# Kernel optimization log

Measured on AMD Instinct MI355X. Metric: run time of the kernel, lower is better.

Reference implementation:

```python
import jax, jax.numpy as jnp
import numpy as np


def setup_inputs() -> dict:
    key = jax.random.key(0)
    k1, k2, k3 = jax.random.split(key, 3)
    B, C, H, W = 16, 512, 64, 64
    K = 32
    std = 1.0 / (K * C) ** 0.5
    x = jax.random.normal(k1, (B, C, H, W), dtype=jnp.float32)
    codewords = jax.random.uniform(k2, (K, C), dtype=jnp.float32, minval=-std, maxval=std)
    scale = jax.random.uniform(k3, (K,), dtype=jnp.float32, minval=-1.0, maxval=0.0)
    return {"x": x, "codewords": codewords, "scale": scale}


def reference(x, codewords, scale):
    # x: [B, C, H, W] -> tokens [B, N, C] with N = H*W
    B, C, H, W = x.shape
    xf = x.reshape(B, C, H * W).transpose(0, 2, 1)  # [B, N, C]

    # (avoids materializing the [B, N, K, C] tensor the torch code builds)
    x_sq = jnp.sum(xf * xf, axis=-1)                 # [B, N]
    c_sq = jnp.sum(codewords * codewords, axis=-1)   # [K]
    xc = jnp.einsum('bnc,kc->bnk', xf, codewords)    # [B, N, K]
    scaled_l2 = scale * (x_sq[..., None] - 2.0 * xc + c_sq)  # [B, N, K]

    w = jax.nn.softmax(scaled_l2, axis=2)            # [B, N, K]

    # aggregate: sum_n w[b,n,k] * (x[b,n,:] - c[k,:])
    #          = einsum(w, x) - (sum_n w) * c
    enc = jnp.einsum('bnk,bnc->bkc', w, xf) - jnp.sum(w, axis=1)[..., None] * codewords
    return enc  # [B, K, C]
```

## Files before the change

kernel.cpp:

```cpp
#include <hip/hip_runtime.h>


#define B_ 16
#define C_ 512
#define N_ 4096
#define K_ 32
#define CHUNK 64
#define NCH (N_ / CHUNK)
#define NBLK (B_ * NCH)
#define XCP 72
#define WLS 40

typedef __attribute__((ext_vector_type(8))) short short8;
typedef __attribute__((ext_vector_type(16))) float floatx16;

__device__ inline unsigned short f2bf(float f) {
    union { float f; unsigned u; } v; v.f = f;
    unsigned r = v.u + 0x7FFFu + ((v.u >> 16) & 1u);
    return (unsigned short)(r >> 16);
}

__global__ __launch_bounds__(256)
void cw_convert(const float* __restrict__ cw, unsigned short* __restrict__ cwb,
                float* __restrict__ csq)
{
    const int tid = threadIdx.x;
    const int k = tid >> 3, q = tid & 7;
    const float4* src = (const float4*)(cw + k * C_ + q * 64);
    float s = 0.f;
    #pragma unroll
    for (int i = 0; i < 16; ++i) {
        const float4 v = src[i];
        s += v.x*v.x + v.y*v.y + v.z*v.z + v.w*v.w;
        const unsigned lo = (unsigned)f2bf(v.x) | ((unsigned)f2bf(v.y) << 16);
        const unsigned hi = (unsigned)f2bf(v.z) | ((unsigned)f2bf(v.w) << 16);
        *(uint2*)&cwb[k * C_ + q * 64 + i * 4] = make_uint2(lo, hi);
    }
    s += __shfl_xor(s, 1); s += __shfl_xor(s, 2); s += __shfl_xor(s, 4);
    if (q == 0) csq[k] = s;
}

template <int USE_WS>
__global__ __launch_bounds__(256, 2)
void enc_kernel(const float* __restrict__ x,
                const unsigned short* __restrict__ cwb,
                const float* __restrict__ csqg,
                const float* __restrict__ cw,
                const float* __restrict__ scale,
                float* __restrict__ outp)
{
    __shared__ unsigned short XC[C_ * XCP];
    __shared__ unsigned short Wl[2][K_ * WLS];
    __shared__ float xsqp[4][CHUNK];
    __shared__ float csq[K_];
    __shared__ float scl[K_];

    const int tid  = threadIdx.x;
    const int wave = tid >> 6;
    const int lane = tid & 63;
    const int l31  = lane & 31;
    const int lh   = lane >> 5;

    const int b     = blockIdx.x >> 6;
    const int chunk = blockIdx.x & (NCH - 1);
    const float* xb = x + (long)b * C_ * N_;

    const int r = tid >> 4;
    const int p = tid & 15;
    const float* xrow = xb + chunk * CHUNK + p * 4;

    if (tid < K_) { scl[tid] = scale[tid]; csq[tid] = csqg[tid]; }

    float4 s0[4], s1[4], s2[4];
#define XISSUE(buf_, g_)                                                       \
    { _Pragma("unroll")                                                        \
      for (int i = 0; i < 4; ++i)                                              \
          buf_[i] = *(const float4*)(xrow + (long)((g_) * 64 + i * 16 + r) * N_); }

    float xs0 = 0.f, xs1 = 0.f, xs2 = 0.f, xs3 = 0.f;
#define XWRITE(buf_, g_)                                                       \
    { _Pragma("unroll")                                                        \
      for (int i = 0; i < 4; ++i) {                                            \
          const float4 v = buf_[i];                                            \
          xs0 += v.x * v.x; xs1 += v.y * v.y;                                  \
          xs2 += v.z * v.z; xs3 += v.w * v.w;                                  \
          const unsigned lo = (unsigned)f2bf(v.x) | ((unsigned)f2bf(v.y) << 16);\
          const unsigned hi = (unsigned)f2bf(v.z) | ((unsigned)f2bf(v.w) << 16);\
          *(uint2*)&XC[((g_) * 64 + i * 16 + r) * XCP + p * 4] = make_uint2(lo, hi);\
      } }

    const unsigned short* cwr = cwb + l31 * C_ + lh * 8;
    short8 afA[4], afB[4];
#define AFLOAD(buf_, g_)                                                       \
    { _Pragma("unroll")                                                        \
      for (int s = 0; s < 4; ++s)                                              \
          buf_[s] = *(const short8*)(cwr + (g_) * 64 + s * 16); }

    XISSUE(s0, 0)
    XISSUE(s1, 1)
    if (wave < 2) AFLOAD(afA, 0)
    XWRITE(s0, 0)
    XISSUE(s2, 2)
    __syncthreads();

    floatx16 S;
    #pragma unroll
    for (int i = 0; i < 16; ++i) S[i] = 0.f;

    #pragma unroll
    for (int g = 0; g < 8; ++g) {
        if (g + 3 < 8) {
            if      ((g % 3) == 0) XISSUE(s0, g + 3)
            else if ((g % 3) == 1) XISSUE(s1, g + 3)
            else                   XISSUE(s2, g + 3)
        }
        if (wave < 2) {
            if (g + 1 < 8) {
                if (g & 1) AFLOAD(afA, g + 1) else AFLOAD(afB, g + 1)
            }
            #pragma unroll
            for (int s = 0; s < 4; ++s) {
                short8 bx;
                #pragma unroll
                for (int j = 0; j < 8; ++j)
                    bx[j] = (short)XC[(g * 64 + s * 16 + lh * 8 + j) * XCP + wave * 32 + l31];
                S = __builtin_amdgcn_mfma_f32_32x32x16_bf16((g & 1) ? afB[s] : afA[s],
                                                            bx, S, 0, 0, 0);
            }
        }
        if (g + 1 < 8) {
            if      (((g + 1) % 3) == 0) XWRITE(s0, g + 1)
            else if (((g + 1) % 3) == 1) XWRITE(s1, g + 1)
            else                         XWRITE(s2, g + 1)
        }
        if (g < 7) __syncthreads();
    }

    xs0 += __shfl_xor(xs0, 16); xs1 += __shfl_xor(xs1, 16);
    xs2 += __shfl_xor(xs2, 16); xs3 += __shfl_xor(xs3, 16);
    xs0 += __shfl_xor(xs0, 32); xs1 += __shfl_xor(xs1, 32);
    xs2 += __shfl_xor(xs2, 32); xs3 += __shfl_xor(xs3, 32);
    if (lane < 16) {
        xsqp[wave][lane * 4 + 0] = xs0; xsqp[wave][lane * 4 + 1] = xs1;
        xsqp[wave][lane * 4 + 2] = xs2; xsqp[wave][lane * 4 + 3] = xs3;
    }
    __syncthreads();

    if (wave < 2) {
        const int n = wave * 32 + l31;
        const float xq = xsqp[0][n] + xsqp[1][n] + xsqp[2][n] + xsqp[3][n];
        float L[16], mx = -3.4e38f;
        #pragma unroll
        for (int rr = 0; rr < 16; ++rr) {
            const int k = (rr & 3) + 8 * (rr >> 2) + 4 * lh;
            L[rr] = scl[k] * (xq - 2.f * S[rr] + csq[k]);
            mx = fmaxf(mx, L[rr]);
        }
        mx = fmaxf(mx, __shfl_xor(mx, 32));
        float sum = 0.f;
        #pragma unroll
        for (int rr = 0; rr < 16; ++rr) { L[rr] = __expf(L[rr] - mx); sum += L[rr]; }
        sum += __shfl_xor(sum, 32);
        const float inv = 1.f / sum;
        #pragma unroll
        for (int rr = 0; rr < 16; ++rr) {
            const int k = (rr & 3) + 8 * (rr >> 2) + 4 * lh;
            Wl[wave][k * WLS + l31] = f2bf(L[rr] * inv);
        }
    }
    __syncthreads();

    short8 aw[4];
    #pragma unroll
    for (int s = 0; s < 4; ++s)
        aw[s] = *(const short8*)&Wl[s >> 1][l31 * WLS + (s & 1) * 16 + lh * 8];

    floatx16 wacc;
    #pragma unroll
    for (int i = 0; i < 16; ++i) wacc[i] = 0.f;
    {
        short8 ones;
        #pragma unroll
        for (int j = 0; j < 8; ++j) ones[j] = (short)0x3F80;
        #pragma unroll
        for (int s = 0; s < 4; ++s)
            wacc = __builtin_amdgcn_mfma_f32_32x32x16_bf16(aw[s], ones, wacc, 0, 0, 0);
    }

    floatx16 acc[4];
    #pragma unroll
    for (int t = 0; t < 4; ++t)
        #pragma unroll
        for (int i = 0; i < 16; ++i) acc[t][i] = 0.f;

    #pragma unroll
    for (int t = 0; t < 4; ++t) {
        const int c = wave * 128 + t * 32 + l31;
        #pragma unroll
        for (int s = 0; s < 4; ++s) {
            const short8 bx = *(const short8*)&XC[c * XCP + s * 16 + lh * 8];
            acc[t] = __builtin_amdgcn_mfma_f32_32x32x16_bf16(aw[s], bx, acc[t], 0, 0, 0);
        }
    }

    float* dst = USE_WS ? (outp + (size_t)blockIdx.x * K_ * C_)
                        : (outp + (size_t)b * K_ * C_);
    #pragma unroll
    for (int t = 0; t < 4; ++t) {
        const int c = wave * 128 + t * 32 + l31;
        #pragma unroll
        for (int rr = 0; rr < 16; ++rr) {
            const int k = (rr & 3) + 8 * (rr >> 2) + 4 * lh;
            const float val = acc[t][rr] - wacc[rr] * cw[k * C_ + c];
            if (USE_WS) dst[k * C_ + c] = val;
            else        atomicAdd(dst + k * C_ + c, val);
        }
    }
}

__global__ __launch_bounds__(256)
void reduce_kernel(const float4* __restrict__ part, float4* __restrict__ out)
{
    const int gid = blockIdx.x * 256 + threadIdx.x;
    const int bb  = gid >> 12;
    const int i4  = gid & 4095;
    const float4* p = part + ((size_t)bb * NCH) * 4096 + i4;
    float4 s = make_float4(0.f, 0.f, 0.f, 0.f);
    #pragma unroll 8
    for (int ch = 0; ch < NCH; ++ch) {
        const float4 v = p[(size_t)ch * 4096];
        s.x += v.x; s.y += v.y; s.z += v.z; s.w += v.w;
    }
    out[gid] = s;
}

extern "C" void kernel_launch(void* const* d_in, const int* in_sizes, int n_in,
                              void* d_out, int out_size, void* d_ws, size_t ws_size,
                              hipStream_t stream) {
    const float* x     = (const float*)d_in[0];
    const float* cw    = (const float*)d_in[1];
    const float* scale = (const float*)d_in[2];
    float* out = (float*)d_out;

    unsigned short* cwb = (unsigned short*)d_ws;
    float* csq = (float*)((char*)d_ws + (size_t)K_ * C_ * sizeof(unsigned short));
    const size_t part_off = 65536;
    const size_t ws_need = part_off + (size_t)NBLK * K_ * C_ * sizeof(float);

    if (ws_size >= ws_need) {
        float* part = (float*)((char*)d_ws + part_off);
        hipLaunchKernelGGL(cw_convert, dim3(1), dim3(256), 0, stream, cw, cwb, csq);
        hipLaunchKernelGGL(enc_kernel<1>, dim3(NBLK), dim3(256), 0, stream,
                           x, cwb, csq, cw, scale, part);
        hipLaunchKernelGGL(reduce_kernel, dim3(256), dim3(256), 0, stream,
                           (const float4*)part, (float4*)out);
    } else {
        hipMemsetAsync(out, 0, (size_t)out_size * sizeof(float), stream);
        hipLaunchKernelGGL(cw_convert, dim3(1), dim3(256), 0, stream, cw, cwb, csq);
        hipLaunchKernelGGL(enc_kernel<0>, dim3(NBLK), dim3(256), 0, stream,
                           x, cwb, csq, cw, scale, out);
    }
}
```

Before: 222.9 us.

## Process two token chunks per block and fold codeword conversion into main kernel

```diff
diff --git a/kernel.cpp b/kernel.cpp
--- a/kernel.cpp
+++ b/kernel.cpp
@@ -6,8 +6,9 @@
 #define N_ 4096
 #define K_ 32
 #define CHUNK 64
-#define NCH (N_ / CHUNK)
-#define NBLK (B_ * NCH)
+#define CPB 2
+#define BPB (N_ / (CHUNK * CPB))
+#define NBLK (B_ * BPB)
 #define XCP 72
 #define WLS 40
 
@@ -20,31 +21,16 @@
     return (unsigned short)(r >> 16);
 }
 
-__global__ __launch_bounds__(256)
-void cw_convert(const float* __restrict__ cw, unsigned short* __restrict__ cwb,
-                float* __restrict__ csq)
-{
-    const int tid = threadIdx.x;
-    const int k = tid >> 3, q = tid & 7;
-    const float4* src = (const float4*)(cw + k * C_ + q * 64);
-    float s = 0.f;
-    #pragma unroll
-    for (int i = 0; i < 16; ++i) {
-        const float4 v = src[i];
-        s += v.x*v.x + v.y*v.y + v.z*v.z + v.w*v.w;
-        const unsigned lo = (unsigned)f2bf(v.x) | ((unsigned)f2bf(v.y) << 16);
-        const unsigned hi = (unsigned)f2bf(v.z) | ((unsigned)f2bf(v.w) << 16);
-        *(uint2*)&cwb[k * C_ + q * 64 + i * 4] = make_uint2(lo, hi);
-    }
-    s += __shfl_xor(s, 1); s += __shfl_xor(s, 2); s += __shfl_xor(s, 4);
-    if (q == 0) csq[k] = s;
+__device__ inline void cbar() {
+    __builtin_amdgcn_sched_barrier(0);
+    asm volatile("s_waitcnt lgkmcnt(0)" ::: "memory");
+    __builtin_amdgcn_s_barrier();
+    __builtin_amdgcn_sched_barrier(0);
 }
 
 template <int USE_WS>
 __global__ __launch_bounds__(256, 2)
 void enc_kernel(const float* __restrict__ x,
-                const unsigned short* __restrict__ cwb,
-                const float* __restrict__ csqg,
                 const float* __restrict__ cw,
                 const float* __restrict__ scale,
                 float* __restrict__ outp)
@@ -61,23 +47,20 @@
     const int l31  = lane & 31;
     const int lh   = lane >> 5;
 
-    const int b     = blockIdx.x >> 6;
-    const int chunk = blockIdx.x & (NCH - 1);
+    const int b    = blockIdx.x >> 5;
+    const int pair = blockIdx.x & (BPB - 1);
     const float* xb = x + (long)b * C_ * N_;
 
     const int r = tid >> 4;
     const int p = tid & 15;
-    const float* xrow = xb + chunk * CHUNK + p * 4;
-
-    if (tid < K_) { scl[tid] = scale[tid]; csq[tid] = csqg[tid]; }
 
     float4 s0[4], s1[4], s2[4];
-#define XISSUE(buf_, g_)                                                       \
+#define XISSUE(buf_, ch_, g_)                                                  \
     { _Pragma("unroll")                                                        \
       for (int i = 0; i < 4; ++i)                                              \
-          buf_[i] = *(const float4*)(xrow + (long)((g_) * 64 + i * 16 + r) * N_); }
-
-    float xs0 = 0.f, xs1 = 0.f, xs2 = 0.f, xs3 = 0.f;
+          buf_[i] = *(const float4*)(xb + (long)((g_) * 64 + i * 16 + r) * N_  \
+                                     + (pair * CPB + (ch_)) * CHUNK + p * 4); }
+
 #define XWRITE(buf_, g_)                                                       \
     { _Pragma("unroll")                                                        \
       for (int i = 0; i < 4; ++i) {                                            \
@@ -89,118 +72,155 @@
           *(uint2*)&XC[((g_) * 64 + i * 16 + r) * XCP + p * 4] = make_uint2(lo, hi);\
       } }
 
-    const unsigned short* cwr = cwb + l31 * C_ + lh * 8;
+    const float* cwr = cw + l31 * C_ + lh * 8;
     short8 afA[4], afB[4];
-#define AFLOAD(buf_, g_)                                                       \
+#define AFLOADG(buf_, g_)                                                      \
     { _Pragma("unroll")                                                        \
-      for (int s = 0; s < 4; ++s)                                              \
-          buf_[s] = *(const short8*)(cwr + (g_) * 64 + s * 16); }
-
-    XISSUE(s0, 0)
-    XISSUE(s1, 1)
-    if (wave < 2) AFLOAD(afA, 0)
-    XWRITE(s0, 0)
-    XISSUE(s2, 2)
-    __syncthreads();
-
-    floatx16 S;
-    #pragma unroll
-    for (int i = 0; i < 16; ++i) S[i] = 0.f;
-
-    #pragma unroll
-    for (int g = 0; g < 8; ++g) {
-        if (g + 3 < 8) {
-            if      ((g % 3) == 0) XISSUE(s0, g + 3)
-            else if ((g % 3) == 1) XISSUE(s1, g + 3)
-            else                   XISSUE(s2, g + 3)
-        }
+      for (int s = 0; s < 4; ++s) {                                            \
+          const float4 u0 = *(const float4*)(cwr + (g_) * 64 + s * 16);        \
+          const float4 u1 = *(const float4*)(cwr + (g_) * 64 + s * 16 + 4);    \
+          short8 t_;                                                           \
+          t_[0] = (short)f2bf(u0.x); t_[1] = (short)f2bf(u0.y);                \
+          t_[2] = (short)f2bf(u0.z); t_[3] = (short)f2bf(u0.w);                \
+          t_[4] = (short)f2bf(u1.x); t_[5] = (short)f2bf(u1.y);                \
+          t_[6] = (short)f2bf(u1.z); t_[7] = (short)f2bf(u1.w);                \
+          buf_[s] = t_; } }
+
+    floatx16 acc[4], wacc;
+    #pragma unroll
+    for (int t = 0; t < 4; ++t)
+        #pragma unroll
+        for (int i = 0; i < 16; ++i) acc[t][i] = 0.f;
+    #pragma unroll
+    for (int i = 0; i < 16; ++i) wacc[i] = 0.f;
+
+    #pragma unroll
+    for (int ch = 0; ch < CPB; ++ch) {
+        float xs0 = 0.f, xs1 = 0.f, xs2 = 0.f, xs3 = 0.f;
+
+        if (ch == 0) {
+            XISSUE(s0, 0, 0)
+            XISSUE(s1, 0, 1)
+            if (tid < K_) scl[tid] = scale[tid];
+            {
+                const int k = tid >> 3, q = tid & 7;
+                const float4* src = (const float4*)(cw + k * C_ + q * 64);
+                float ssum = 0.f;
+                #pragma unroll
+                for (int i = 0; i < 16; ++i) {
+                    const float4 v = src[i];
+                    ssum += v.x*v.x + v.y*v.y + v.z*v.z + v.w*v.w;
+                }
+                ssum += __shfl_xor(ssum, 1);
+                ssum += __shfl_xor(ssum, 2);
+                ssum += __shfl_xor(ssum, 4);
+                if (q == 0) csq[k] = ssum;
+            }
+            if (wave < 2) AFLOADG(afA, 0)
+            XWRITE(s0, 0)
+            XISSUE(s2, 0, 2)
+        } else {
+            if (wave < 2) AFLOADG(afA, 0)
+            XWRITE(s0, 0)
+        }
+        cbar();
+
+        floatx16 S;
+        #pragma unroll
+        for (int i = 0; i < 16; ++i) S[i] = 0.f;
+
+        #pragma unroll
+        for (int g = 0; g < 8; ++g) {
+            if (g + 3 < 8) {
+                if      ((g % 3) == 0) XISSUE(s0, ch, g + 3)
+                else if ((g % 3) == 1) XISSUE(s1, ch, g + 3)
+                else                   XISSUE(s2, ch, g + 3)
+            }
+            if (wave < 2) {
+                if (g + 1 < 8) {
+                    if (g & 1) AFLOADG(afA, g + 1) else AFLOADG(afB, g + 1)
+                }
+                #pragma unroll
+                for (int s = 0; s < 4; ++s) {
+                    short8 bx;
+                    #pragma unroll
+                    for (int j = 0; j < 8; ++j)
+                        bx[j] = (short)XC[(g * 64 + s * 16 + lh * 8 + j) * XCP
+                                          + wave * 32 + l31];
+                    S = __builtin_amdgcn_mfma_f32_32x32x16_bf16(
+                            (g & 1) ? afB[s] : afA[s], bx, S, 0, 0, 0);
+                }
+            }
+            if (g + 1 < 8) {
+                if      (((g + 1) % 3) == 0) XWRITE(s0, g + 1)
+                else if (((g + 1) % 3) == 1) XWRITE(s1, g + 1)
+                else                         XWRITE(s2, g + 1)
+            } else if (ch + 1 < CPB) {
+                XISSUE(s0, ch + 1, 0)
+                XISSUE(s1, ch + 1, 1)
+                XISSUE(s2, ch + 1, 2)
+            }
+            cbar();
+        }
+
+        xs0 += __shfl_xor(xs0, 16); xs1 += __shfl_xor(xs1, 16);
+        xs2 += __shfl_xor(xs2, 16); xs3 += __shfl_xor(xs3, 16);
+        xs0 += __shfl_xor(xs0, 32); xs1 += __shfl_xor(xs1, 32);
+        xs2 += __shfl_xor(xs2, 32); xs3 += __shfl_xor(xs3, 32);
+        if (lane < 16) {
+            xsqp[wave][lane * 4 + 0] = xs0; xsqp[wave][lane * 4 + 1] = xs1;
+            xsqp[wave][lane * 4 + 2] = xs2; xsqp[wave][lane * 4 + 3] = xs3;
+        }
+        cbar();
+
         if (wave < 2) {
-            if (g + 1 < 8) {
-                if (g & 1) AFLOAD(afA, g + 1) else AFLOAD(afB, g + 1)
-            }
+            const int n = wave * 32 + l31;
+            const float xq = xsqp[0][n] + xsqp[1][n] + xsqp[2][n] + xsqp[3][n];
+            float L[16], mx = -3.4e38f;
+            #pragma unroll
+            for (int rr = 0; rr < 16; ++rr) {
+                const int k = (rr & 3) + 8 * (rr >> 2) + 4 * lh;
+                L[rr] = scl[k] * (xq - 2.f * S[rr] + csq[k]);
+                mx = fmaxf(mx, L[rr]);
+            }
+            mx = fmaxf(mx, __shfl_xor(mx, 32));
+            float sum = 0.f;
+            #pragma unroll
+            for (int rr = 0; rr < 16; ++rr) { L[rr] = __expf(L[rr] - mx); sum += L[rr]; }
+            sum += __shfl_xor(sum, 32);
+            const float inv = 1.f / sum;
+            #pragma unroll
+            for (int rr = 0; rr < 16; ++rr) {
+                const int k = (rr & 3) + 8 * (rr >> 2) + 4 * lh;
+                Wl[wave][k * WLS + l31] = f2bf(L[rr] * inv);
+            }
+        }
+        cbar();
+
+        short8 aw[4];
+        #pragma unroll
+        for (int s = 0; s < 4; ++s)
+            aw[s] = *(const short8*)&Wl[s >> 1][l31 * WLS + (s & 1) * 16 + lh * 8];
+
+        {
+            short8 ones;
+            #pragma unroll
+            for (int j = 0; j < 8; ++j) ones[j] = (short)0x3F80;
+            #pragma unroll
+            for (int s = 0; s < 4; ++s)
+                wacc = __builtin_amdgcn_mfma_f32_32x32x16_bf16(aw[s], ones, wacc, 0, 0, 0);
+        }
+
+        #pragma unroll
+        for (int t = 0; t < 4; ++t) {
+            const int c = wave * 128 + t * 32 + l31;
             #pragma unroll
             for (int s = 0; s < 4; ++s) {
-                short8 bx;
-                #pragma unroll
-                for (int j = 0; j < 8; ++j)
-                    bx[j] = (short)XC[(g * 64 + s * 16 + lh * 8 + j) * XCP + wave * 32 + l31];
-                S = __builtin_amdgcn_mfma_f32_32x32x16_bf16((g & 1) ? afB[s] : afA[s],
-                                                            bx, S, 0, 0, 0);
-            }
-        }
-        if (g + 1 < 8) {
-            if      (((g + 1) % 3) == 0) XWRITE(s0, g + 1)
-            else if (((g + 1) % 3) == 1) XWRITE(s1, g + 1)
-            else                         XWRITE(s2, g + 1)
-        }
-        if (g < 7) __syncthreads();
-    }
-
-    xs0 += __shfl_xor(xs0, 16); xs1 += __shfl_xor(xs1, 16);
-    xs2 += __shfl_xor(xs2, 16); xs3 += __shfl_xor(xs3, 16);
-    xs0 += __shfl_xor(xs0, 32); xs1 += __shfl_xor(xs1, 32);
-    xs2 += __shfl_xor(xs2, 32); xs3 += __shfl_xor(xs3, 32);
-    if (lane < 16) {
-        xsqp[wave][lane * 4 + 0] = xs0; xsqp[wave][lane * 4 + 1] = xs1;
-        xsqp[wave][lane * 4 + 2] = xs2; xsqp[wave][lane * 4 + 3] = xs3;
-    }
-    __syncthreads();
-
-    if (wave < 2) {
-        const int n = wave * 32 + l31;
-        const float xq = xsqp[0][n] + xsqp[1][n] + xsqp[2][n] + xsqp[3][n];
-        float L[16], mx = -3.4e38f;
-        #pragma unroll
-        for (int rr = 0; rr < 16; ++rr) {
-            const int k = (rr & 3) + 8 * (rr >> 2) + 4 * lh;
-            L[rr] = scl[k] * (xq - 2.f * S[rr] + csq[k]);
-            mx = fmaxf(mx, L[rr]);
-        }
-        mx = fmaxf(mx, __shfl_xor(mx, 32));
-        float sum = 0.f;
-        #pragma unroll
-        for (int rr = 0; rr < 16; ++rr) { L[rr] = __expf(L[rr] - mx); sum += L[rr]; }
-        sum += __shfl_xor(sum, 32);
-        const float inv = 1.f / sum;
-        #pragma unroll
-        for (int rr = 0; rr < 16; ++rr) {
-            const int k = (rr & 3) + 8 * (rr >> 2) + 4 * lh;
-            Wl[wave][k * WLS + l31] = f2bf(L[rr] * inv);
-        }
-    }
-    __syncthreads();
-
-    short8 aw[4];
-    #pragma unroll
-    for (int s = 0; s < 4; ++s)
-        aw[s] = *(const short8*)&Wl[s >> 1][l31 * WLS + (s & 1) * 16 + lh * 8];
-
-    floatx16 wacc;
-    #pragma unroll
-    for (int i = 0; i < 16; ++i) wacc[i] = 0.f;
-    {
-        short8 ones;
-        #pragma unroll
-        for (int j = 0; j < 8; ++j) ones[j] = (short)0x3F80;
-        #pragma unroll
-        for (int s = 0; s < 4; ++s)
-            wacc = __builtin_amdgcn_mfma_f32_32x32x16_bf16(aw[s], ones, wacc, 0, 0, 0);
-    }
-
-    floatx16 acc[4];
-    #pragma unroll
-    for (int t = 0; t < 4; ++t)
-        #pragma unroll
-        for (int i = 0; i < 16; ++i) acc[t][i] = 0.f;
-
-    #pragma unroll
-    for (int t = 0; t < 4; ++t) {
-        const int c = wave * 128 + t * 32 + l31;
-        #pragma unroll
-        for (int s = 0; s < 4; ++s) {
-            const short8 bx = *(const short8*)&XC[c * XCP + s * 16 + lh * 8];
-            acc[t] = __builtin_amdgcn_mfma_f32_32x32x16_bf16(aw[s], bx, acc[t], 0, 0, 0);
-        }
+                const short8 bx = *(const short8*)&XC[c * XCP + s * 16 + lh * 8];
+                acc[t] = __builtin_amdgcn_mfma_f32_32x32x16_bf16(aw[s], bx, acc[t], 0, 0, 0);
+            }
+        }
+        if (ch + 1 < CPB) cbar();
     }
 
     float* dst = USE_WS ? (outp + (size_t)blockIdx.x * K_ * C_)
@@ -224,11 +244,11 @@
     const int gid = blockIdx.x * 256 + threadIdx.x;
     const int bb  = gid >> 12;
     const int i4  = gid & 4095;
-    const float4* p = part + ((size_t)bb * NCH) * 4096 + i4;
+    const float4* pp = part + ((size_t)bb * BPB) * 4096 + i4;
     float4 s = make_float4(0.f, 0.f, 0.f, 0.f);
     #pragma unroll 8
-    for (int ch = 0; ch < NCH; ++ch) {
-        const float4 v = p[(size_t)ch * 4096];
+    for (int j = 0; j < BPB; ++j) {
+        const float4 v = pp[(size_t)j * 4096];
         s.x += v.x; s.y += v.y; s.z += v.z; s.w += v.w;
     }
     out[gid] = s;
@@ -242,22 +262,16 @@
     const float* scale = (const float*)d_in[2];
     float* out = (float*)d_out;
 
-    unsigned short* cwb = (unsigned short*)d_ws;
-    float* csq = (float*)((char*)d_ws + (size_t)K_ * C_ * sizeof(unsigned short));
-    const size_t part_off = 65536;
-    const size_t ws_need = part_off + (size_t)NBLK * K_ * C_ * sizeof(float);
-
+    const size_t ws_need = (size_t)NBLK * K_ * C_ * sizeof(float);
     if (ws_size >= ws_need) {
-        float* part = (float*)((char*)d_ws + part_off);
-        hipLaunchKernelGGL(cw_convert, dim3(1), dim3(256), 0, stream, cw, cwb, csq);
+        float* part = (float*)d_ws;
         hipLaunchKernelGGL(enc_kernel<1>, dim3(NBLK), dim3(256), 0, stream,
-                           x, cwb, csq, cw, scale, part);
+                           x, cw, scale, part);
         hipLaunchKernelGGL(reduce_kernel, dim3(256), dim3(256), 0, stream,
                            (const float4*)part, (float4*)out);
     } else {
         hipMemsetAsync(out, 0, (size_t)out_size * sizeof(float), stream);
-        hipLaunchKernelGGL(cw_convert, dim3(1), dim3(256), 0, stream, cw, cwb, csq);
         hipLaunchKernelGGL(enc_kernel<0>, dim3(NBLK), dim3(256), 0, stream,
-                           x, cwb, csq, cw, scale, out);
-    }
-}
+                           x, cw, scale, out);
+    }
+}
```

Measured after the change: 227.5 us. +2.1%, slower.
